# Kernel tuning notes

Hardware: AMD Instinct MI355X
Metric: run time of the kernel (lower is better)

## Reference

```python
import jax, jax.numpy as jnp
import numpy as np

N, B, E, H, G, L = 128, 2, 512, 1024, 50, 3
RBF_RADIUS = 12.0
AVG_LEN = 60.0


def _resmlp(h, Win, bin_, Wh, bh, Wout, bout):
    # input proj + activation, residual hidden blocks, linear head
    h = jax.nn.gelu(h @ Win + bin_, approximate=False)
    for i in range(Wh.shape[0]):  # fixed small number of layers
        h = h + jax.nn.gelu(h @ Wh[i] + bh[i], approximate=False)
    return h @ Wout + bout


def setup_inputs() -> dict:
    key = jax.random.key(0)
    ks = jax.random.split(key, 20)
    s_in = 1.0 / np.sqrt(3 * E)
    s_h = 1.0 / np.sqrt(H)
    s_g = 1.0 / np.sqrt(G)
    return {
        'x': jax.random.normal(ks[0], (N, B, E), jnp.float32),
        'dist': jax.random.uniform(ks[1], (N, N, B), jnp.float32),
        'vec_hat': jax.random.normal(ks[2], (N, N, B, 3), jnp.float32),
        'mask': jnp.ones((B, N), dtype=bool),
        'rbf_W': jax.random.normal(ks[3], (G, E), jnp.float32) * s_g,
        'rbf_b': jnp.zeros((E,), jnp.float32),
        'e_Win': jax.random.normal(ks[4], (3 * E, H), jnp.float32) * s_in,
        'e_bin': jnp.zeros((H,), jnp.float32),
        'e_Wh': jax.random.normal(ks[5], (L, H, H), jnp.float32) * s_h,
        'e_bh': jnp.zeros((L, H), jnp.float32),
        'e_Wout': jax.random.normal(ks[6], (H, 1), jnp.float32) * s_h,
        'e_bout': jnp.zeros((1,), jnp.float32),
        'f_Win': jax.random.normal(ks[7], (3 * E, H), jnp.float32) * s_in,
        'f_bin': jnp.zeros((H,), jnp.float32),
        'f_Wh': jax.random.normal(ks[8], (L, H, H), jnp.float32) * s_h,
        'f_bh': jnp.zeros((L, H), jnp.float32),
        'f_Wout': jax.random.normal(ks[9], (H, 1), jnp.float32) * s_h,
        'f_bout': jnp.zeros((1,), jnp.float32),
    }


def reference(x, dist, vec_hat, mask, rbf_W, rbf_b, e_Win, e_bin, e_Wh, e_bh,
              e_Wout, e_bout, f_Win, f_bin, f_Wh, f_bh, f_Wout, f_bout):
    # Gaussian RBF expansion + linear projection to embed_dim
    offset = jnp.linspace(0.0, RBF_RADIUS, G)
    coeff = -0.5 / (offset[1] - offset[0]) ** 2
    g = jnp.exp(coeff * (dist[..., None] - offset) ** 2)       # (N,N,B,G)
    rbf = g @ rbf_W + rbf_b                                    # (N,N,B,E)

    # all-pairs concat feature: [x_i, x_j, rbf_ij]  -> (N,N,B,3E)
    feat = jnp.concatenate([
        jnp.broadcast_to(x[:, None], rbf.shape),
        jnp.broadcast_to(x[None, :], rbf.shape),
        rbf,
    ], axis=-1)

    entries = (mask.T[:, None] & mask.T[None, :])[..., None].astype(feat.dtype)  # (N,N,B,1)

    energy_pairs = _resmlp(feat, e_Win, e_bin, e_Wh, e_bh, e_Wout, e_bout)       # (N,N,B,1)
    force_pairs = _resmlp(feat, f_Win, f_bin, f_Wh, f_bh, f_Wout, f_bout) * vec_hat  # (N,N,B,3)

    energy = (energy_pairs * entries).sum((0, 1)) / AVG_LEN ** 2  # (B,1)
    forces = (force_pairs * entries).sum(0) / AVG_LEN             # (N,B,3)
    # torch: forces.transpose(0,1)[mask]; mask is all-True here, so this is a reshape
    forces = jnp.swapaxes(forces, 0, 1).reshape(-1, 3)            # (B*N,3)
    return energy, forces
```

## Files before the change

kernel.cpp:

```cpp
#include <hip/hip_runtime.h>
#include <stdint.h>

typedef __bf16 bf16x8 __attribute__((ext_vector_type(8)));
typedef __bf16 bf16x4 __attribute__((ext_vector_type(4)));
typedef float  f32x4  __attribute__((ext_vector_type(4)));
typedef unsigned int u32;

__device__ __forceinline__ void gl_lds16(const void* gptr, void* lptr) {
    __builtin_amdgcn_global_load_lds(
        (const __attribute__((address_space(1))) u32*)gptr,
        (__attribute__((address_space(3))) u32*)lptr,
        16, 0, 0);
}

__device__ __forceinline__ float gelu_f(float x) {
    float u = 0.7978845608f * x * (1.0f + 0.044715f * x * x);
    float e = __expf(2.0f * u);
    float t = 1.0f - 2.0f / (e + 1.0f);
    return 0.5f * x * (1.0f + t);
}

#define MEMFENCE __asm__ __volatile__("" ::: "memory")

__global__ void zero_out(float* __restrict__ o, int n) {
    int i = blockIdx.x * 256 + threadIdx.x;
    if (i < n) o[i] = 0.0f;
}

__global__ __launch_bounds__(256)
void transpose_multi(const float* __restrict__ src0, const float* __restrict__ src1,
                     __bf16* __restrict__ dst0, __bf16* __restrict__ dst1,
                     int K, int Ncols, int perBranch) {
    const int z = blockIdx.z;
    const int branch = z / perBranch;
    const int l = z - branch * perBranch;
    const size_t elems = (size_t)K * Ncols;
    const float* src = (branch ? src1 : src0) + (size_t)l * elems;
    __bf16* dst = (branch ? dst1 : dst0) + (size_t)l * elems;

    __shared__ float tile[64][65];
    const int bk = blockIdx.x * 64;
    const int bn = blockIdx.y * 64;
    const int tid = threadIdx.x;
    const int tr = tid >> 4;
    const int tc = (tid & 15) * 4;
#pragma unroll
    for (int p = 0; p < 4; ++p) {
        const int r = tr + p * 16;
        float4 v = *(const float4*)&src[(size_t)(bk + r) * Ncols + bn + tc];
        tile[r][tc] = v.x; tile[r][tc + 1] = v.y;
        tile[r][tc + 2] = v.z; tile[r][tc + 3] = v.w;
    }
    __syncthreads();
#pragma unroll
    for (int p = 0; p < 4; ++p) {
        const int rn = tr + p * 16;
        bf16x4 o;
        o[0] = (__bf16)tile[tc + 0][rn];
        o[1] = (__bf16)tile[tc + 1][rn];
        o[2] = (__bf16)tile[tc + 2][rn];
        o[3] = (__bf16)tile[tc + 3][rn];
        *(bf16x4*)&dst[(size_t)(bn + rn) * K + bk + tc] = o;
    }
}

__global__ void f32_to_bf16(const float* __restrict__ s, __bf16* __restrict__ d, int n) {
    int idx = blockIdx.x * 256 + threadIdx.x;
    if (idx * 4 < n) {
        float4 v = *(const float4*)(s + idx * 4);
        bf16x4 o;
        o[0] = (__bf16)v.x; o[1] = (__bf16)v.y; o[2] = (__bf16)v.z; o[3] = (__bf16)v.w;
        *(bf16x4*)(d + idx * 4) = o;
    }
}

__global__ void build_M1(const float* __restrict__ rbfW, const float* __restrict__ rbf_b,
                         __bf16* __restrict__ M1) {
    int t = blockIdx.x * 256 + threadIdx.x;
    int r = t >> 8;
    int c = (t & 255) * 2;
    float v0 = 0.f, v1 = 0.f;
    if (r < 50)       { v0 = rbfW[r * 512 + c]; v1 = rbfW[r * 512 + c + 1]; }
    else if (r == 50) { v0 = rbf_b[c];          v1 = rbf_b[c + 1]; }
    M1[r * 512 + c] = (__bf16)v0;
    M1[r * 512 + c + 1] = (__bf16)v1;
}

__global__ __launch_bounds__(256)
void build_G(const float* __restrict__ dist, __bf16* __restrict__ G) {
    const int t = threadIdx.x;
    const int row = blockIdx.x * 32 + (t >> 3);
    const int c0 = (t & 7) * 8;
    const float sp = 12.0f / 49.0f;
    const float coeff = -0.5f / (sp * sp);
    const float d = dist[row];
    bf16x8 v;
#pragma unroll
    for (int q = 0; q < 8; ++q) {
        const int k = c0 + q;
        float val;
        if (k < 50)       { float tt = d - (float)k * sp; val = __expf(coeff * tt * tt); }
        else if (k == 50) val = 1.0f;
        else              val = 0.0f;
        v[q] = (__bf16)val;
    }
    *(bf16x8*)(G + (size_t)row * 64 + c0) = v;
}

template <int NK, int NBN, int MODE, bool DUAL, int MINW, bool SWZ>
__global__ __launch_bounds__(256, MINW)
void gemm_k(const __bf16* __restrict__ A0, const __bf16* __restrict__ A1,
            const __bf16* __restrict__ B0, const __bf16* __restrict__ B1,
            int lda, int ldb, int ldc,
            const float* __restrict__ bias0, const float* __restrict__ bias1,
            __bf16* __restrict__ C0, __bf16* __restrict__ C1,
            float* __restrict__ Cf0, float* __restrict__ Cf1,
            const float* __restrict__ P0, const float* __restrict__ P1,
            const float* __restrict__ wout0, const float* __restrict__ wout1,
            float* __restrict__ dot0, float* __restrict__ dot1) {
    constexpr int NBS = (NBN == 16) ? 4 : (NBN == 8) ? 3 : 0;
    __shared__ __align__(16) __bf16 As[3][128 * 32];
    __shared__ __align__(16) __bf16 Bs[3][128 * 32];

    const int tid = threadIdx.x;
    int bn, bm, branch = 0;
    if constexpr (SWZ) {
        const int x = blockIdx.x & 7;
        const int slot = blockIdx.x >> 3;
        bn = slot & (NBN - 1);
        int grp = x + ((slot >> NBS) << 3);
        if constexpr (DUAL) {
            const int half = (gridDim.x >> NBS) >> 1;
            branch = (grp >= half);
            if (branch) grp -= half;
        }
        bm = grp;
    } else {
        int f2 = blockIdx.x;
        if constexpr (DUAL) {
            const int half = gridDim.x >> 1;
            branch = (f2 >= half);
            if (branch) f2 -= half;
        }
        bn = f2 & (NBN - 1);
        bm = f2 >> NBS;
    }
    const int w = tid >> 6;
    const int lane = tid & 63;

    const __bf16* Ab = (DUAL && branch) ? A1 : A0;
    const __bf16* Bb = (DUAL && branch) ? B1 : B0;

    const int r0 = tid >> 2;
    const int s0 = tid & 3;
    const char* gA0 = (const char*)Ab + (size_t)(bm * 128 + r0) * lda + s0 * 16;
    const char* gA1 = gA0 + (size_t)64 * lda;
    const char* gB0 = (const char*)Bb + (size_t)(bn * 128 + r0) * ldb + s0 * 16;
    const char* gB1 = gB0 + (size_t)64 * ldb;

    char* lA0 = (char*)&As[0][0] + w * 1024;
    char* lA1 = (char*)&As[1][0] + w * 1024;
    char* lA2 = (char*)&As[2][0] + w * 1024;
    char* lB0 = (char*)&Bs[0][0] + w * 1024;
    char* lB1 = (char*)&Bs[1][0] + w * 1024;
    char* lB2 = (char*)&Bs[2][0] + w * 1024;

    const int wm = (w >> 1) & 1;
    const int wn = w & 1;
    const int lm = lane & 15;
    const int ko = (lane >> 4) << 3;
    const int fo = (wm * 64 + lm) * 32 + ko;
    const int go = (wn * 64 + lm) * 32 + ko;
    const __bf16* pA0 = &As[0][0] + fo;
    const __bf16* pA1 = &As[1][0] + fo;
    const __bf16* pA2 = &As[2][0] + fo;
    const __bf16* pB0 = &Bs[0][0] + go;
    const __bf16* pB1 = &Bs[1][0] + go;
    const __bf16* pB2 = &Bs[2][0] + go;

    f32x4 acc[4][4];
    const f32x4 zero = {0.0f, 0.0f, 0.0f, 0.0f};
#pragma unroll
    for (int i = 0; i < 4; ++i)
#pragma unroll
        for (int j = 0; j < 4; ++j) acc[i][j] = zero;

    auto stage = [&](int buf) {
        char* la = (buf == 0) ? lA0 : (buf == 1) ? lA1 : lA2;
        char* lb = (buf == 0) ? lB0 : (buf == 1) ? lB1 : lB2;
        gl_lds16(gA0, la); gl_lds16(gA1, la + 4096);
        gl_lds16(gB0, lb); gl_lds16(gB1, lb + 4096);
        gA0 += 64; gA1 += 64; gB0 += 64; gB1 += 64;
    };
    auto compute = [&](int buf) {
        const __bf16* pa = (buf == 0) ? pA0 : (buf == 1) ? pA1 : pA2;
        const __bf16* pb = (buf == 0) ? pB0 : (buf == 1) ? pB1 : pB2;
        bf16x8 af[4], bfg[4];
#pragma unroll
        for (int i = 0; i < 4; ++i) {
            af[i]  = *(const bf16x8*)(pa + i * 512);
            bfg[i] = *(const bf16x8*)(pb + i * 512);
        }
#pragma unroll
        for (int mi = 0; mi < 4; ++mi)
#pragma unroll
            for (int ni = 0; ni < 4; ++ni)
                acc[mi][ni] = __builtin_amdgcn_mfma_f32_16x16x32_bf16(
                    af[mi], bfg[ni], acc[mi][ni], 0, 0, 0);
    };
    auto iterstep = [&](int cbuf, int sbuf) {
        MEMFENCE;
        __builtin_amdgcn_s_waitcnt(0xF74);
        __builtin_amdgcn_s_barrier();
        MEMFENCE;
        compute(cbuf);
        MEMFENCE;
        stage(sbuf);
        MEMFENCE;
    };

    stage(0);
    stage(1);
    constexpr int NIT = NK - 2;
    constexpr int NG = NIT / 3;
    constexpr int NR = NIT % 3;
    for (int g = 0; g < NG; ++g) {
        iterstep(0, 2);
        iterstep(1, 0);
        iterstep(2, 1);
    }
    if constexpr (NR >= 1) iterstep(0, 2);
    if constexpr (NR >= 2) iterstep(1, 0);
    MEMFENCE;
    __builtin_amdgcn_s_waitcnt(0xF74);
    __builtin_amdgcn_s_barrier();
    MEMFENCE;
    compute((NK - 2) % 3);
    MEMFENCE;
    __builtin_amdgcn_s_waitcnt(0xF70);
    __builtin_amdgcn_s_barrier();
    MEMFENCE;
    compute((NK - 1) % 3);

    const int col0 = bn * 128 + wn * 64 + lm;
    const int row0 = bm * 128 + wm * 64 + ((lane >> 4) << 2);
    const int ldaE = lda >> 1;

    float rowdot[16];
    if constexpr (MODE == 1) {
#pragma unroll
        for (int q = 0; q < 16; ++q) rowdot[q] = 0.0f;
    }

    const bool side = (MODE == 2) && (bn >= 8);
    const float* bp = (MODE == 2) ? (side ? bias1 : bias0)
                                  : ((DUAL && branch) ? bias1 : bias0);
    __bf16* Cout = (MODE == 2) ? (side ? C1 : C0)
                               : ((DUAL && branch) ? C1 : C0);
    const float* woutb = (MODE == 1) ? ((DUAL && branch) ? wout1 : wout0) : nullptr;

#pragma unroll
    for (int ni = 0; ni < 4; ++ni) {
        const int gn = col0 + ni * 16;
        const int gnl = (MODE == 2) ? (gn & 1023) : gn;
        float bv = 0.0f;
        if constexpr (MODE <= 2) bv = bp[gnl];
        float wv = 0.0f;
        if constexpr (MODE == 1) wv = woutb[gn];

        float res[16];
        if constexpr (MODE == 0 || MODE == 1) {
#pragma unroll
            for (int mi = 0; mi < 4; ++mi)
#pragma unroll
                for (int rr = 0; rr < 4; ++rr)
                    res[mi * 4 + rr] =
                        (float)Ab[(size_t)(row0 + mi * 16 + rr) * ldaE + gn];
        } else if constexpr (MODE == 2) {
#pragma unroll
            for (int mi = 0; mi < 4; ++mi)
#pragma unroll
                for (int rr = 0; rr < 4; ++rr) {
                    const int gm = row0 + mi * 16 + rr;
                    const int p0row = ((gm >> 8) << 1) | (gm & 1);
                    const int p1row = gm & 255;
                    res[mi * 4 + rr] = P0[(size_t)p0row * 2048 + gn]
                                     + P1[(size_t)p1row * 2048 + gn];
                }
        }
        MEMFENCE;

#pragma unroll
        for (int mi = 0; mi < 4; ++mi) {
#pragma unroll
            for (int rr = 0; rr < 4; ++rr) {
                const int gm = row0 + mi * 16 + rr;
                const float a = acc[mi][ni][rr];
                if constexpr (MODE == 0) {
                    float v = gelu_f(a + bv) + res[mi * 4 + rr];
                    Cout[(size_t)gm * ldc + gn] = (__bf16)v;
                } else if constexpr (MODE == 1) {
                    float v = gelu_f(a + bv) + res[mi * 4 + rr];
                    rowdot[mi * 4 + rr] += v * wv;
                } else if constexpr (MODE == 2) {
                    float v = a + bv + res[mi * 4 + rr];
                    Cout[(size_t)gm * ldc + gnl] = (__bf16)gelu_f(v);
                } else if constexpr (MODE == 3) {
                    float* Cfw = (DUAL && branch) ? Cf1 : Cf0;
                    Cfw[(size_t)gm * ldc + gn] = a;
                } else {
                    C0[(size_t)gm * ldc + gn] = (__bf16)a;
                }
            }
        }
    }

    if constexpr (MODE == 1) {
#pragma unroll
        for (int s = 1; s < 16; s <<= 1)
#pragma unroll
            for (int q = 0; q < 16; ++q) rowdot[q] += __shfl_xor(rowdot[q], s);
        if (lm == 0) {
            float* dotb = (DUAL && branch) ? dot1 : dot0;
            float* dp = dotb + (size_t)(bn * 2 + wn) * 32768 + row0;
#pragma unroll
            for (int q = 0; q < 16; ++q)
                dp[(q >> 2) * 16 + (q & 3)] = rowdot[q];
        }
    }
}

__global__ __launch_bounds__(128)
void finalize(const float* __restrict__ dot_e, const float* __restrict__ dot_f,
              const float* __restrict__ eb, const float* __restrict__ fb,
              const float* __restrict__ vec, float* __restrict__ out) {
    const int bj = blockIdx.x;
    const int bb = bj >> 7, jj = bj & 127;
    const int i = threadIdx.x;
    const int m = (i * 128 + jj) * 2 + bb;
    float e = eb[0], f = fb[0];
#pragma unroll
    for (int s = 0; s < 16; ++s) {
        e += dot_e[(size_t)s * 32768 + m];
        f += dot_f[(size_t)s * 32768 + m];
    }
    f *= (1.0f / 60.0f);
    float fx = f * vec[(size_t)m * 3 + 0];
    float fy = f * vec[(size_t)m * 3 + 1];
    float fz = f * vec[(size_t)m * 3 + 2];
#pragma unroll
    for (int off = 32; off > 0; off >>= 1) {
        e  += __shfl_down(e, off);
        fx += __shfl_down(fx, off);
        fy += __shfl_down(fy, off);
        fz += __shfl_down(fz, off);
    }
    __shared__ float red[2][4];
    const int wv = i >> 6, lane = i & 63;
    if (lane == 0) { red[wv][0] = e; red[wv][1] = fx; red[wv][2] = fy; red[wv][3] = fz; }
    __syncthreads();
    if (i == 0) {
        atomicAdd(&out[bb], (red[0][0] + red[1][0]) * (1.0f / 3600.0f));
        float* fo = out + 2 + bj * 3;
        fo[0] = red[0][1] + red[1][1];
        fo[1] = red[0][2] + red[1][2];
        fo[2] = red[0][3] + red[1][3];
    }
}

extern "C" void kernel_launch(void* const* d_in, const int* in_sizes, int n_in,
                              void* d_out, int out_size, void* d_ws, size_t ws_size,
                              hipStream_t stream) {
    const float* x     = (const float*)d_in[0];
    const float* dist  = (const float*)d_in[1];
    const float* vec   = (const float*)d_in[2];
    const float* rbfW  = (const float*)d_in[4];
    const float* rbf_b = (const float*)d_in[5];
    const float* eWin  = (const float*)d_in[6];
    const float* ebin  = (const float*)d_in[7];
    const float* eWh   = (const float*)d_in[8];
    const float* ebh   = (const float*)d_in[9];
    const float* eWout = (const float*)d_in[10];
    const float* ebout = (const float*)d_in[11];
    const float* fWin  = (const float*)d_in[12];
    const float* fbin  = (const float*)d_in[13];
    const float* fWh   = (const float*)d_in[14];
    const float* fbh   = (const float*)d_in[15];
    const float* fWout = (const float*)d_in[16];
    const float* fbout = (const float*)d_in[17];
    float* out = (float*)d_out;

    char* p = (char*)d_ws;
    __bf16* WinTcat = (__bf16*)p;
    __bf16* eWinT = WinTcat;          p += (size_t)1024 * 1536 * 2;
    __bf16* fWinT = (__bf16*)p;       p += (size_t)1024 * 1536 * 2;
    __bf16* eWhT0 = (__bf16*)p;       p += (size_t)3 * 1024 * 1024 * 2;
    __bf16* fWhT0 = (__bf16*)p;       p += (size_t)3 * 1024 * 1024 * 2;
    __bf16* xb  = (__bf16*)p;         p += (size_t)256 * 512 * 2;
    __bf16* M1  = (__bf16*)p;         p += (size_t)128 * 512 * 2;
    __bf16* WgT = (__bf16*)p;         p += (size_t)2048 * 128 * 2;
    __bf16* G   = (__bf16*)p;         p += (size_t)32768 * 64 * 2;
    float* P0   = (float*)p;          p += (size_t)256 * 2048 * 4;
    float* P1   = (float*)p;          p += (size_t)256 * 2048 * 4;
    float* dot_e = (float*)p;         p += (size_t)16 * 32768 * 4;
    float* dot_f = (float*)p;         p += (size_t)16 * 32768 * 4;
    const size_t SLAB = (size_t)32768 * 1024 * 2;
    __bf16* he0 = (__bf16*)p;         p += SLAB;
    __bf16* hf0 = (__bf16*)p;         p += SLAB;
    __bf16* hAe = (__bf16*)p;         p += SLAB;
    __bf16* hAf = hAe;
    const bool dualHidden = ((size_t)(p - (char*)d_ws) + SLAB) <= ws_size;
    if (dualHidden) hAf = (__bf16*)p;

    zero_out<<<dim3(4), dim3(256), 0, stream>>>(out, 770);

    transpose_multi<<<dim3(24, 16, 2), dim3(256), 0, stream>>>(
        eWin, fWin, eWinT, fWinT, 1536, 1024, 1);
    transpose_multi<<<dim3(16, 16, 6), dim3(256), 0, stream>>>(
        eWh, fWh, eWhT0, fWhT0, 1024, 1024, 3);
    f32_to_bf16<<<dim3(128), dim3(256), 0, stream>>>(x, xb, 131072);
    build_M1<<<dim3(128), dim3(256), 0, stream>>>(rbfW, rbf_b, M1);
    build_G<<<dim3(1024), dim3(256), 0, stream>>>(dist, G);

    const dim3 blk(256);
    gemm_k<16, 16, 3, true, 3, false><<<dim3(64), blk, 0, stream>>>(
        xb, xb, WinTcat, WinTcat + 512, 1024, 3072, 2048,
        nullptr, nullptr, nullptr, nullptr, P0, P1,
        nullptr, nullptr, nullptr, nullptr, nullptr, nullptr);
    gemm_k<16, 1, 4, false, 3, false><<<dim3(16), blk, 0, stream>>>(
        WinTcat + 1024, nullptr, M1, nullptr, 3072, 1024, 128,
        nullptr, nullptr, WgT, nullptr, nullptr, nullptr,
        nullptr, nullptr, nullptr, nullptr, nullptr, nullptr);
    gemm_k<2, 16, 2, false, 3, true><<<dim3(4096), blk, 0, stream>>>(
        G, nullptr, WgT, nullptr, 128, 256, 1024,
        ebin, fbin, he0, hf0, nullptr, nullptr, P0, P1,
        nullptr, nullptr, nullptr, nullptr);

    if (dualHidden) {
        gemm_k<32, 8, 0, true, 3, true><<<dim3(4096), blk, 0, stream>>>(
            he0, hf0, eWhT0, fWhT0, 2048, 2048, 1024,
            ebh + 0, fbh + 0, hAe, hAf, nullptr, nullptr,
            nullptr, nullptr, nullptr, nullptr, nullptr, nullptr);
        gemm_k<32, 8, 0, true, 3, true><<<dim3(4096), blk, 0, stream>>>(
            hAe, hAf, eWhT0 + (size_t)1048576, fWhT0 + (size_t)1048576,
            2048, 2048, 1024, ebh + 1024, fbh + 1024, he0, hf0,
            nullptr, nullptr, nullptr, nullptr, nullptr, nullptr, nullptr, nullptr);
    } else {
        gemm_k<32, 8, 0, false, 3, true><<<dim3(2048), blk, 0, stream>>>(
            he0, nullptr, eWhT0, nullptr, 2048, 2048, 1024,
            ebh + 0, nullptr, hAe, nullptr, nullptr, nullptr,
            nullptr, nullptr, nullptr, nullptr, nullptr, nullptr);
        gemm_k<32, 8, 0, false, 3, true><<<dim3(2048), blk, 0, stream>>>(
            hAe, nullptr, eWhT0 + (size_t)1048576, nullptr, 2048, 2048, 1024,
            ebh + 1024, nullptr, he0, nullptr, nullptr, nullptr,
            nullptr, nullptr, nullptr, nullptr, nullptr, nullptr);
        gemm_k<32, 8, 0, false, 3, true><<<dim3(2048), blk, 0, stream>>>(
            hf0, nullptr, fWhT0, nullptr, 2048, 2048, 1024,
            fbh + 0, nullptr, hAf, nullptr, nullptr, nullptr,
            nullptr, nullptr, nullptr, nullptr, nullptr, nullptr);
        gemm_k<32, 8, 0, false, 3, true><<<dim3(2048), blk, 0, stream>>>(
            hAf, nullptr, fWhT0 + (size_t)1048576, nullptr, 2048, 2048, 1024,
            fbh + 1024, nullptr, hf0, nullptr, nullptr, nullptr,
            nullptr, nullptr, nullptr, nullptr, nullptr, nullptr);
    }
    gemm_k<32, 8, 1, true, 2, true><<<dim3(4096), blk, 0, stream>>>(
        he0, hf0, eWhT0 + (size_t)2 * 1048576, fWhT0 + (size_t)2 * 1048576,
        2048, 2048, 1024, ebh + 2048, fbh + 2048,
        nullptr, nullptr, nullptr, nullptr, nullptr, nullptr,
        eWout, fWout, dot_e, dot_f);

    finalize<<<dim3(256), dim3(128), 0, stream>>>(dot_e, dot_f, ebout, fbout, vec, out);
}
```

Before: 805.6 us.

## Add 256x256-tile double-buffered GEMM kernel for residual MLP hidden layers

Adds a new 512-thread GEMM kernel with 256x256 output tiles, XOR-swizzled LDS and two-stage double buffering via direct global-to-LDS loads. It uses it for all three hidden residual layers of both MLP branches, with the fused GELU, residual and output-dot epilogue. The larger tiles aim to raise operand reuse and MFMA density and cut global traffic. The cost is 128KB of LDS per block, which limits occupancy to about one block per CU, and a heavy register load from the 8x4 accumulators.

```diff
diff --git a/kernel.cpp b/kernel.cpp
--- a/kernel.cpp
+++ b/kernel.cpp
@@ -326,6 +326,197 @@
 #pragma unroll
             for (int q = 0; q < 16; ++q)
                 dp[(q >> 2) * 16 + (q & 3)] = rowdot[q];
+        }
+    }
+}
+
+template <int MODE, bool DUAL>
+__global__ __launch_bounds__(512, 2)
+void gemm256(const __bf16* __restrict__ A0, const __bf16* __restrict__ A1,
+             const __bf16* __restrict__ B0, const __bf16* __restrict__ B1,
+             const float* __restrict__ bias0, const float* __restrict__ bias1,
+             __bf16* __restrict__ C0, __bf16* __restrict__ C1,
+             const float* __restrict__ wout0, const float* __restrict__ wout1,
+             float* __restrict__ dot0, float* __restrict__ dot1) {
+    __shared__ __align__(16) char ldsbuf[131072];
+
+    const int tid = threadIdx.x;
+    const int nxg = gridDim.x >> 3;
+    const int id = (blockIdx.x & 7) * nxg + (blockIdx.x >> 3);
+    const int bn = id & 3;
+    int rest = id >> 2;
+    int branch = 0;
+    if constexpr (DUAL) { branch = rest >> 7; rest &= 127; }
+    const int bm = rest;
+
+    const __bf16* __restrict__ Ab = (DUAL && branch) ? A1 : A0;
+    const __bf16* __restrict__ Bb = (DUAL && branch) ? B1 : B0;
+
+    const int w = tid >> 6;
+    const int lane = tid & 63;
+
+    const int srow = tid >> 3;
+    const int scol = ((tid & 7) * 16) ^ (((tid >> 3) & 7) << 4);
+    const char* gA = (const char*)Ab + (size_t)(bm * 256 + srow) * 2048 + scol;
+    const char* gB = (const char*)Bb + (size_t)(bn * 256 + srow) * 2048 + scol;
+    char* stBase = ldsbuf + w * 1024;
+
+    auto stageTile = [&](int kt, int buf) {
+        const size_t ko = (size_t)kt * 128;
+        char* d = stBase + buf * 65536;
+        gl_lds16(gA + ko,              d);
+        gl_lds16(gA + ko +  64 * 2048, d + 8192);
+        gl_lds16(gA + ko + 128 * 2048, d + 16384);
+        gl_lds16(gA + ko + 192 * 2048, d + 24576);
+        gl_lds16(gB + ko,              d + 32768);
+        gl_lds16(gB + ko +  64 * 2048, d + 40960);
+        gl_lds16(gB + ko + 128 * 2048, d + 49152);
+        gl_lds16(gB + ko + 192 * 2048, d + 57344);
+    };
+
+    const int wm = w >> 2, wn = w & 3;
+    const int lm = lane & 15, lq = lane >> 4;
+    const int xorm = (lm & 7) << 4;
+    const int rA0 = (wm * 128 + lm) * 128;
+    const int rB0 = 32768 + (wn * 64 + lm) * 128;
+    const int offk0 = (lq * 16) ^ xorm;
+    const int offk1 = (64 + lq * 16) ^ xorm;
+
+    f32x4 acc[8][4];
+    const f32x4 zero = {0.0f, 0.0f, 0.0f, 0.0f};
+#pragma unroll
+    for (int i = 0; i < 8; ++i)
+#pragma unroll
+        for (int j = 0; j < 4; ++j) acc[i][j] = zero;
+
+    auto body = [&](int kt, bool last) {
+        const char* Lb = ldsbuf + (kt & 1) * 65536;
+        MEMFENCE;
+        if (last) __builtin_amdgcn_s_waitcnt(0xF70);
+        else      __builtin_amdgcn_s_waitcnt(0xF78);
+        __builtin_amdgcn_s_barrier();
+        MEMFENCE;
+        bf16x8 a0[8], b0[4], a1[8], b1[4];
+#pragma unroll
+        for (int mi = 0; mi < 8; ++mi)
+            a0[mi] = *(const bf16x8*)(Lb + rA0 + mi * 2048 + offk0);
+#pragma unroll
+        for (int ni = 0; ni < 4; ++ni)
+            b0[ni] = *(const bf16x8*)(Lb + rB0 + ni * 2048 + offk0);
+        __builtin_amdgcn_s_setprio(1);
+#pragma unroll
+        for (int mi = 0; mi < 4; ++mi)
+#pragma unroll
+            for (int ni = 0; ni < 4; ++ni)
+                acc[mi][ni] = __builtin_amdgcn_mfma_f32_16x16x32_bf16(
+                    a0[mi], b0[ni], acc[mi][ni], 0, 0, 0);
+        __builtin_amdgcn_s_setprio(0);
+#pragma unroll
+        for (int mi = 0; mi < 8; ++mi)
+            a1[mi] = *(const bf16x8*)(Lb + rA0 + mi * 2048 + offk1);
+#pragma unroll
+        for (int ni = 0; ni < 4; ++ni)
+            b1[ni] = *(const bf16x8*)(Lb + rB0 + ni * 2048 + offk1);
+        __builtin_amdgcn_s_setprio(1);
+#pragma unroll
+        for (int mi = 4; mi < 8; ++mi)
+#pragma unroll
+            for (int ni = 0; ni < 4; ++ni)
+                acc[mi][ni] = __builtin_amdgcn_mfma_f32_16x16x32_bf16(
+                    a0[mi], b0[ni], acc[mi][ni], 0, 0, 0);
+        __builtin_amdgcn_s_setprio(0);
+        MEMFENCE;
+        __builtin_amdgcn_s_waitcnt(0xC07F);
+        __builtin_amdgcn_s_barrier();
+        MEMFENCE;
+        if (!last && kt < 14) stageTile(kt + 2, kt & 1);
+        MEMFENCE;
+        __builtin_amdgcn_s_setprio(1);
+#pragma unroll
+        for (int mi = 0; mi < 4; ++mi)
+#pragma unroll
+            for (int ni = 0; ni < 4; ++ni)
+                acc[mi][ni] = __builtin_amdgcn_mfma_f32_16x16x32_bf16(
+                    a1[mi], b1[ni], acc[mi][ni], 0, 0, 0);
+#pragma unroll
+        for (int mi = 4; mi < 8; ++mi)
+#pragma unroll
+            for (int ni = 0; ni < 4; ++ni)
+                acc[mi][ni] = __builtin_amdgcn_mfma_f32_16x16x32_bf16(
+                    a1[mi], b1[ni], acc[mi][ni], 0, 0, 0);
+        __builtin_amdgcn_s_setprio(0);
+    };
+
+    stageTile(0, 0);
+    stageTile(1, 1);
+    for (int kt = 0; kt < 15; ++kt) body(kt, false);
+    body(15, true);
+
+    const int row0 = bm * 256 + wm * 128 + lq * 4;
+    const int col0 = bn * 256 + wn * 64 + lm;
+    const float* __restrict__ bp = (DUAL && branch) ? bias1 : bias0;
+    float bv[4];
+#pragma unroll
+    for (int ni = 0; ni < 4; ++ni) bv[ni] = bp[col0 + ni * 16];
+
+    if constexpr (MODE == 0) {
+        __bf16* __restrict__ Cw = (DUAL && branch) ? C1 : C0;
+#pragma unroll
+        for (int mi = 0; mi < 8; ++mi) {
+            float res[16];
+#pragma unroll
+            for (int ni = 0; ni < 4; ++ni)
+#pragma unroll
+                for (int rr = 0; rr < 4; ++rr)
+                    res[ni * 4 + rr] =
+                        (float)Ab[(size_t)(row0 + mi * 16 + rr) * 1024 + col0 + ni * 16];
+            MEMFENCE;
+#pragma unroll
+            for (int ni = 0; ni < 4; ++ni)
+#pragma unroll
+                for (int rr = 0; rr < 4; ++rr) {
+                    float v = gelu_f(acc[mi][ni][rr] + bv[ni]) + res[ni * 4 + rr];
+                    Cw[(size_t)(row0 + mi * 16 + rr) * 1024 + col0 + ni * 16] = (__bf16)v;
+                }
+        }
+    } else {
+        const float* __restrict__ wb = (DUAL && branch) ? wout1 : wout0;
+        float wv[4];
+#pragma unroll
+        for (int ni = 0; ni < 4; ++ni) wv[ni] = wb[col0 + ni * 16];
+        float rowdot[32];
+#pragma unroll
+        for (int q = 0; q < 32; ++q) rowdot[q] = 0.0f;
+#pragma unroll
+        for (int mi = 0; mi < 8; ++mi) {
+            float res[16];
+#pragma unroll
+            for (int ni = 0; ni < 4; ++ni)
+#pragma unroll
+                for (int rr = 0; rr < 4; ++rr)
+                    res[ni * 4 + rr] =
+                        (float)Ab[(size_t)(row0 + mi * 16 + rr) * 1024 + col0 + ni * 16];
+            MEMFENCE;
+#pragma unroll
+            for (int ni = 0; ni < 4; ++ni)
+#pragma unroll
+                for (int rr = 0; rr < 4; ++rr) {
+                    float v = gelu_f(acc[mi][ni][rr] + bv[ni]) + res[ni * 4 + rr];
+                    rowdot[mi * 4 + rr] += v * wv[ni];
+                }
+        }
+#pragma unroll
+        for (int s = 1; s < 16; s <<= 1)
+#pragma unroll
+            for (int q = 0; q < 32; ++q) rowdot[q] += __shfl_xor(rowdot[q], s);
+        if (lm == 0) {
+            float* __restrict__ db = (DUAL && branch) ? dot1 : dot0;
+            float* dp = db + (size_t)(bn * 4 + wn) * 32768 + bm * 256 + wm * 128;
+#pragma unroll
+            for (int mi = 0; mi < 8; ++mi)
+#pragma unroll
+                for (int rr = 0; rr < 4; ++rr)
+                    dp[mi * 16 + lq * 4 + rr] = rowdot[mi * 4 + rr];
         }
     }
 }
@@ -436,38 +627,38 @@
         ebin, fbin, he0, hf0, nullptr, nullptr, P0, P1,
         nullptr, nullptr, nullptr, nullptr);
 
+    const dim3 blk512(512);
     if (dualHidden) {
-        gemm_k<32, 8, 0, true, 3, true><<<dim3(4096), blk, 0, stream>>>(
-            he0, hf0, eWhT0, fWhT0, 2048, 2048, 1024,
-            ebh + 0, fbh + 0, hAe, hAf, nullptr, nullptr,
-            nullptr, nullptr, nullptr, nullptr, nullptr, nullptr);
-        gemm_k<32, 8, 0, true, 3, true><<<dim3(4096), blk, 0, stream>>>(
+        gemm256<0, true><<<dim3(1024), blk512, 0, stream>>>(
+            he0, hf0, eWhT0, fWhT0, ebh + 0, fbh + 0,
+            hAe, hAf, nullptr, nullptr, nullptr, nullptr);
+        gemm256<0, true><<<dim3(1024), blk512, 0, stream>>>(
             hAe, hAf, eWhT0 + (size_t)1048576, fWhT0 + (size_t)1048576,
-            2048, 2048, 1024, ebh + 1024, fbh + 1024, he0, hf0,
-            nullptr, nullptr, nullptr, nullptr, nullptr, nullptr, nullptr, nullptr);
+            ebh + 1024, fbh + 1024, he0, hf0, nullptr, nullptr, nullptr, nullptr);
+        gemm256<1, true><<<dim3(1024), blk512, 0, stream>>>(
+            he0, hf0, eWhT0 + (size_t)2 * 1048576, fWhT0 + (size_t)2 * 1048576,
+            ebh + 2048, fbh + 2048, nullptr, nullptr,
+            eWout, fWout, dot_e, dot_f);
     } else {
-        gemm_k<32, 8, 0, false, 3, true><<<dim3(2048), blk, 0, stream>>>(
-            he0, nullptr, eWhT0, nullptr, 2048, 2048, 1024,
-            ebh + 0, nullptr, hAe, nullptr, nullptr, nullptr,
-            nullptr, nullptr, nullptr, nullptr, nullptr, nullptr);
-        gemm_k<32, 8, 0, false, 3, true><<<dim3(2048), blk, 0, stream>>>(
-            hAe, nullptr, eWhT0 + (size_t)1048576, nullptr, 2048, 2048, 1024,
-            ebh + 1024, nullptr, he0, nullptr, nullptr, nullptr,
-            nullptr, nullptr, nullptr, nullptr, nullptr, nullptr);
-        gemm_k<32, 8, 0, false, 3, true><<<dim3(2048), blk, 0, stream>>>(
-            hf0, nullptr, fWhT0, nullptr, 2048, 2048, 1024,
-            fbh + 0, nullptr, hAf, nullptr, nullptr, nullptr,
-            nullptr, nullptr, nullptr, nullptr, nullptr, nullptr);
-        gemm_k<32, 8, 0, false, 3, true><<<dim3(2048), blk, 0, stream>>>(
-            hAf, nullptr, fWhT0 + (size_t)1048576, nullptr, 2048, 2048, 1024,
-            fbh + 1024, nullptr, hf0, nullptr, nullptr, nullptr,
-            nullptr, nullptr, nullptr, nullptr, nullptr, nullptr);
-    }
-    gemm_k<32, 8, 1, true, 2, true><<<dim3(4096), blk, 0, stream>>>(
-        he0, hf0, eWhT0 + (size_t)2 * 1048576, fWhT0 + (size_t)2 * 1048576,
-        2048, 2048, 1024, ebh + 2048, fbh + 2048,
-        nullptr, nullptr, nullptr, nullptr, nullptr, nullptr,
-        eWout, fWout, dot_e, dot_f);
+        gemm256<0, false><<<dim3(512), blk512, 0, stream>>>(
+            he0, nullptr, eWhT0, nullptr, ebh + 0, nullptr,
+            hAe, nullptr, nullptr, nullptr, nullptr, nullptr);
+        gemm256<0, false><<<dim3(512), blk512, 0, stream>>>(
+            hAe, nullptr, eWhT0 + (size_t)1048576, nullptr, ebh + 1024, nullptr,
+            he0, nullptr, nullptr, nullptr, nullptr, nullptr);
+        gemm256<1, false><<<dim3(512), blk512, 0, stream>>>(
+            he0, nullptr, eWhT0 + (size_t)2 * 1048576, nullptr, ebh + 2048, nullptr,
+            nullptr, nullptr, eWout, nullptr, dot_e, nullptr);
+        gemm256<0, false><<<dim3(512), blk512, 0, stream>>>(
+            hf0, nullptr, fWhT0, nullptr, fbh + 0, nullptr,
+            hAf, nullptr, nullptr, nullptr, nullptr, nullptr);
+        gemm256<0, false><<<dim3(512), blk512, 0, stream>>>(
+            hAf, nullptr, fWhT0 + (size_t)1048576, nullptr, fbh + 1024, nullptr,
+            hf0, nullptr, nullptr, nullptr, nullptr, nullptr);
+        gemm256<1, false><<<dim3(512), blk512, 0, stream>>>(
+            hf0, nullptr, fWhT0 + (size_t)2 * 1048576, nullptr, fbh + 2048, nullptr,
+            nullptr, nullptr, fWout, nullptr, dot_f, nullptr);
+    }
 
     finalize<<<dim3(256), dim3(128), 0, stream>>>(dot_e, dot_f, ebout, fbout, vec, out);
 }
```

New measurement: 716.1 us. 1.12x faster.
